# Kernel tuning notes

Measured on AMD Instinct MI355X. Metric: run time of the kernel, lower is better.

The kernel has to match this reference:

```python
import jax, jax.numpy as jnp
import numpy as np

B, S, T, E, H = 64, 256, 128, 256, 512


def setup_inputs() -> dict:
    key = jax.random.key(0)
    ks = jax.random.split(key, 12)
    sc = 0.05
    return {
        "trg_embed": jax.random.normal(ks[0], (B, T + 1, E), jnp.float32),
        "encoder_hidden": jax.random.normal(ks[1], (B, S, 2 * H), jnp.float32),
        "encoder_final": jax.random.normal(ks[2], (B, H), jnp.float32),
        "src_mask": jnp.ones((B, S), bool),
        "W_ih": jax.random.normal(ks[3], (3 * H, E + 2 * H), jnp.float32) * sc,
        "W_hh": jax.random.normal(ks[4], (3 * H, H), jnp.float32) * sc,
        "b_ih": jnp.zeros((3 * H,), jnp.float32),
        "b_hh": jnp.zeros((3 * H,), jnp.float32),
        "bridge_w": jax.random.normal(ks[5], (H, H), jnp.float32) * sc,
        "bridge_b": jnp.zeros((H,), jnp.float32),
        "key_w": jax.random.normal(ks[6], (H, 2 * H), jnp.float32) * sc,
        "query_w": jax.random.normal(ks[7], (H, H), jnp.float32) * sc,
        "energy_w": jax.random.normal(ks[8], (H,), jnp.float32) * sc,
        "pre_w": jax.random.normal(ks[9], (2 * H, H + 2 * H + E), jnp.float32) * sc,
        "pre_b": jnp.zeros((2 * H,), jnp.float32),
        "max_len": T,
    }


def reference(trg_embed, encoder_hidden, encoder_final, src_mask,
              W_ih, W_hh, b_ih, b_hh, bridge_w, bridge_b,
              key_w, query_w, energy_w, pre_w, pre_b, max_len):
    # bridge: initial decoder state from final encoder state
    h0 = jnp.tanh(encoder_final @ bridge_w.T + bridge_b)          # [B,H]
    # precomputed attention keys
    proj_key = jnp.einsum('bsk,hk->bsh', encoder_hidden, key_w)   # [B,S,H]
    neg = jnp.asarray(-1e9, trg_embed.dtype)

    prev = jnp.swapaxes(trg_embed[:, :max_len], 0, 1)             # [T,B,E]
    curr = jnp.swapaxes(trg_embed[:, 1:max_len + 1], 0, 1)        # [T,B,E] (generate_first)

    def step(h, pc):
        p, c = pc
        # --- additive (Bahdanau) attention, query = current hidden ---
        q = h @ query_w.T                                         # [B,H]
        scores = jnp.tanh(q[:, None, :] + proj_key) @ energy_w    # [B,S]
        scores = jnp.where(src_mask, scores, neg)
        alphas = jax.nn.softmax(scores, axis=-1)                  # [B,S]
        context = jnp.einsum('bs,bsd->bd', alphas, encoder_hidden)  # [B,2H]
        # --- generate_first: pre_output from previous hidden ---
        pre_out = jnp.concatenate([p, h, context], axis=-1) @ pre_w.T + pre_b  # [B,2H]
        # --- GRU cell (torch gate order r, z, n) ---
        x = jnp.concatenate([c, context], axis=-1)                # [B,E+2H]
        gi = x @ W_ih.T + b_ih
        gh = h @ W_hh.T + b_hh
        ir, iz, inn = jnp.split(gi, 3, axis=-1)
        hr, hz, hn = jnp.split(gh, 3, axis=-1)
        r = jax.nn.sigmoid(ir + hr)
        z = jax.nn.sigmoid(iz + hz)
        n = jnp.tanh(inn + r * hn)
        h_new = (1 - z) * n + z * h
        return h_new, (h_new, pre_out, alphas)

    h_fin, (states, pre_outs, attns) = jax.lax.scan(step, h0, (prev, curr))
    return (jnp.swapaxes(states, 0, 1),      # [B,T,H] decoder_states
            h_fin,                            # [B,H] final hidden
            jnp.swapaxes(pre_outs, 0, 1),     # [B,T,2H] pre_output_vectors
            jnp.swapaxes(attns, 0, 1))        # [B,T,S] attention_vectors
```

## Files before the change

### kernel.cpp

```cpp
#include <hip/hip_runtime.h>
#include <hip/hip_fp16.h>

using u32 = unsigned int;

constexpr int B = 64, S = 256, T = 128, E = 256, H = 512, H2 = 1024;
constexpr int TE = (T + 1) * E;

constexpr size_t OUT_HFIN = (size_t)B * T * H;
constexpr size_t OUT_PRE  = OUT_HFIN + (size_t)B * H;
constexpr size_t OUT_ATT  = OUT_PRE + (size_t)B * T * H2;

constexpr size_t WS_HPREV = 0;
constexpr size_t WS_QWT4  = 32768;
constexpr size_t WS_TRGT  = WS_QWT4 + 131072;
constexpr size_t WS_PK2   = WS_TRGT + 1056768;
constexpr size_t WS_HT2R  = WS_PK2 + 4194304;
constexpr size_t WS_QBUF  = WS_HT2R + 129 * 16384;
constexpr size_t WS_CTXR  = WS_QBUF + (size_t)128 * 16384;
constexpr size_t WS_SEWR  = WS_CTXR + (size_t)128 * 32768;
constexpr size_t WS_BAR   = WS_SEWR + 32768;
constexpr size_t WS_WFR   = WS_BAR + 1024;
constexpr size_t WS_TOTAL = WS_WFR + (size_t)192 * 3584 * 4;

constexpr int L_EHS  = 0;
constexpr int L_EW   = 131072;
constexpr int L_HP   = 133376;
constexpr int L_SH2  = 134400;
constexpr int L_QRED = 135424;
constexpr int L_SHQ  = 135424;
constexpr int L_SCP  = 137728;
constexpr int L_SE   = 142080;
constexpr int L_CPAR = 142336;
constexpr int L_CRE1 = 135424;
constexpr int L_CRC  = 139520;
constexpr int L_SST  = 151808;
constexpr int SMEM_BYTES = 155904;

typedef _Float16 half8 __attribute__((ext_vector_type(8)));
typedef float    f32x4 __attribute__((ext_vector_type(4)));
union UH  { u32 u; _Float16 h[2]; };
union UH8 { uint4 v; half8 h; };

__device__ __forceinline__ u32 pkh(float a, float b) {
  auto v = __builtin_amdgcn_cvt_pkrtz(a, b);
  u32 r; __builtin_memcpy(&r, &v, 4); return r;
}
__device__ __forceinline__ float f16lo(u32 u) { UH x; x.u = u; return (float)x.h[0]; }
__device__ __forceinline__ float f16hi(u32 u) { UH x; x.u = u; return (float)x.h[1]; }

#if __has_builtin(__builtin_amdgcn_fdot2)
__device__ __forceinline__ float fdot2(u32 a, u32 b, float c) {
  typedef _Float16 h2t __attribute__((ext_vector_type(2)));
  h2t av, bv; __builtin_memcpy(&av, &a, 4); __builtin_memcpy(&bv, &b, 4);
  return __builtin_amdgcn_fdot2(av, bv, c, false);
}
#else
__device__ __forceinline__ float fdot2(u32 a, u32 b, float c) {
  return c + f16lo(a) * f16lo(b) + f16hi(a) * f16hi(b);
}
#endif

__device__ __forceinline__ float fast_tanh(float x) {
  return 1.0f - 2.0f / (__expf(2.0f * x) + 1.0f);
}
__device__ __forceinline__ float fast_sigmoid(float x) {
  return 1.0f / (1.0f + __expf(-x));
}
__device__ __forceinline__ float dot4(float4 a, float4 b) {
  return a.x * b.x + a.y * b.y + a.z * b.z + a.w * b.w;
}

__device__ __forceinline__ void st_wt(u32* p, u32 v) {
  __hip_atomic_store(p, v, __ATOMIC_RELAXED, __HIP_MEMORY_SCOPE_AGENT);
}
__device__ __forceinline__ void st_wt_f(float* p, float v) {
  union { float f; u32 u; } c; c.f = v;
  __hip_atomic_store((u32*)p, c.u, __ATOMIC_RELAXED, __HIP_MEMORY_SCOPE_AGENT);
}

__device__ __forceinline__ void gbar(u32* bar, int p, u32 n) {
  asm volatile("s_waitcnt vmcnt(0) lgkmcnt(0)" ::: "memory");
  __syncthreads();
  if (threadIdx.x == 0) {
    u32 old = __hip_atomic_fetch_add(bar + (p >> 4) * 32, 1u,
                                     __ATOMIC_RELAXED, __HIP_MEMORY_SCOPE_AGENT);
    if ((old & 15u) == 15u) {
      u32 r = __hip_atomic_fetch_add(bar + 768, 1u,
                                     __ATOMIC_RELAXED, __HIP_MEMORY_SCOPE_AGENT);
      if ((r & 15u) == 15u)
        __hip_atomic_store(bar + 800, n, __ATOMIC_RELAXED, __HIP_MEMORY_SCOPE_AGENT);
    }
    while (__hip_atomic_load(bar + 800, __ATOMIC_RELAXED,
                             __HIP_MEMORY_SCOPE_AGENT) < n)
      __builtin_amdgcn_s_sleep(2);
  }
  __syncthreads();
  asm volatile("" ::: "memory");
}

__global__ void bridge_kernel(const float* __restrict__ ef,
                              const float* __restrict__ bw,
                              const float* __restrict__ bb,
                              float* __restrict__ h0T) {
  int gid = blockIdx.x * blockDim.x + threadIdx.x;
  int j = gid >> 6, b = gid & 63;
  const float4* w = (const float4*)(bw + (size_t)j * H);
  const float4* e = (const float4*)(ef + (size_t)b * H);
  float acc = 0.f;
#pragma unroll 4
  for (int k = 0; k < H / 4; ++k) acc += dot4(w[k], e[k]);
  h0T[gid] = tanhf(acc + bb[j]);
}

__global__ void packh0_kernel(const float* __restrict__ hprevT, u32* __restrict__ hT2) {
  int idx = blockIdx.x * 512 + threadIdx.x;
  int dp = idx >> 6, b = idx & 63;
  hT2[(size_t)(dp >> 2) * 256 + b * 4 + (dp & 3)] =
      pkh(hprevT[(size_t)(2 * dp) * 64 + b], hprevT[(size_t)(2 * dp + 1) * 64 + b]);
}

__global__ void qwt4_kernel(const float* __restrict__ qw, uint4* __restrict__ qwt4) {
  int kq = blockIdx.x, j = threadIdx.x;
  const float* src = qw + (size_t)j * H + kq * 8;
  uint4 o;
  o.x = pkh(src[0], src[1]); o.y = pkh(src[2], src[3]);
  o.z = pkh(src[4], src[5]); o.w = pkh(src[6], src[7]);
  qwt4[(size_t)kq * 512 + j] = o;
}

__global__ void trgT2_kernel(const float* __restrict__ trg, u32* __restrict__ trgT) {
  int b = blockIdx.x, tid = threadIdx.x;
  for (int i = 0; i < 33; ++i) {
    int idx = i * 512 + tid;
    if (idx >= 129 * 128) break;
    int tt = idx >> 7, kp = idx & 127;
    float2 v = *(const float2*)(trg + (size_t)b * TE + (size_t)tt * 256 + kp * 2);
    trgT[(size_t)tt * 8192 + (size_t)(kp >> 2) * 256 + b * 4 + (kp & 3)] = pkh(v.x, v.y);
  }
}

__global__ void wfrag_kernel(const float* __restrict__ W_ih,
                             const float* __restrict__ W_hh,
                             const float* __restrict__ pre_w,
                             uint4* __restrict__ wfr) {
  const int p = blockIdx.x;
  const bool isGate = p < 128;
  for (int idx = threadIdx.x; idx < 56 * 64; idx += 512) {
    int ks = idx >> 6, lane = idx & 63;
    u32 w4[4];
#pragma unroll
    for (int i = 0; i < 4; ++i) {
      int kp = ks * 16 + (lane >> 4) * 4 + i;
      float a = 0.f, bv = 0.f;
      if (isGate) {
        int row = lane & 15, jo = row >> 2, g = row & 3;
        int j = p * 4 + jo;
        if (kp < 128) {
          if (g < 3) { const float* s_ = W_ih + (size_t)(g * 512 + j) * 1280 + kp * 2; a = s_[0]; bv = s_[1]; }
        } else if (kp < 384) {
          int c = (kp - 128) * 2;
          if (g < 2)       { const float* s_ = W_hh + (size_t)(g * 512 + j) * 512 + c; a = s_[0]; bv = s_[1]; }
          else if (g == 3) { const float* s_ = W_hh + (size_t)(1024 + j) * 512 + c;    a = s_[0]; bv = s_[1]; }
        } else {
          if (g < 3) { const float* s_ = W_ih + (size_t)(g * 512 + j) * 1280 + 256 + (kp - 384) * 2; a = s_[0]; bv = s_[1]; }
        }
      } else {
        int row = (p - 128) * 16 + (lane & 15);
        int c = (kp < 128) ? kp * 2 : (kp < 384) ? 256 + (kp - 128) * 2 : 768 + (kp - 384) * 2;
        const float* s_ = pre_w + (size_t)row * 1792 + c;
        a = s_[0]; bv = s_[1];
      }
      w4[i] = pkh(a, bv);
    }
    wfr[(size_t)p * 3584 + idx] = make_uint4(w4[0], w4[1], w4[2], w4[3]);
  }
}

__global__ void __launch_bounds__(256, 4) projkey2_kernel(
    const float* __restrict__ eh, const float* __restrict__ key_w,
    u32* __restrict__ pk) {
  constexpr int ST = 68;
  __shared__ float ea[64][ST];
  __shared__ float kb[64][ST];
  const int b  = blockIdx.x;
  const int s0 = blockIdx.y * 64;
  const int j0 = blockIdx.z * 64;
  const int tid = threadIdx.x;
  const int rl = tid >> 2, ql = tid & 3;
  const int tx = tid & 15, ty = tid >> 4;
  float acc[4][4] = {};
  const float* esrc = eh + ((size_t)b * S + s0 + rl) * H2;
  const float* ksrc = key_w + (size_t)(j0 + rl) * H2;
  for (int kc = 0; kc < H2; kc += 64) {
    float4 ev[4], kv[4];
#pragma unroll
    for (int m = 0; m < 4; ++m) {
      ev[m] = *(const float4*)(esrc + kc + ql * 16 + m * 4);
      kv[m] = *(const float4*)(ksrc + kc + ql * 16 + m * 4);
    }
    __syncthreads();
#pragma unroll
    for (int m = 0; m < 4; ++m) {
#pragma unroll
      for (int c = 0; c < 4; ++c) {
        int k = ql * 16 + m * 4 + c;
        ea[k][rl] = (&ev[m].x)[c];
        kb[k][rl] = (&kv[m].x)[c];
      }
    }
    __syncthreads();
#pragma unroll 8
    for (int k = 0; k < 64; ++k) {
      float4 a4 = *(const float4*)&ea[k][ty * 4];
      float4 b4 = *(const float4*)&kb[k][tx * 4];
      float av[4] = {a4.x, a4.y, a4.z, a4.w};
      float bv[4] = {b4.x, b4.y, b4.z, b4.w};
#pragma unroll
      for (int i = 0; i < 4; ++i)
#pragma unroll
        for (int jj = 0; jj < 4; ++jj) acc[i][jj] += av[i] * bv[jj];
    }
  }
#pragma unroll
  for (int i = 0; i < 4; ++i) {
    int s = s0 + ty * 4 + i;
    u32 u0 = pkh(acc[i][0], acc[i][1]);
    u32 u1 = pkh(acc[i][2], acc[i][3]);
    *(uint2*)(pk + (size_t)(b * S + s) * 256 + j0 / 2 + tx * 2) = make_uint2(u0, u1);
  }
}

#define MFMA_STEP(k, bsrc, kq, acc) do {                                      \
    UH8 a_, b_;                                                               \
    a_.v = wfp[(size_t)(k) * 64];                                             \
    b_.v = *(const uint4*)((bsrc) + (size_t)(((kq) * 4 + g4) * 256 + bcol * 4)); \
    (acc) = __builtin_amdgcn_mfma_f32_16x16x32_f16(a_.h, b_.h, (acc), 0, 0, 0); \
  } while (0)

__global__ void __launch_bounds__(1024) decoder_loop(
    const float* __restrict__ eh,
    const float* __restrict__ b_ih, const float* __restrict__ b_hh,
    const float* __restrict__ energy_w, const float* __restrict__ pre_b,
    float* __restrict__ out, float* __restrict__ ws) {
  __builtin_amdgcn_fence(__ATOMIC_ACQUIRE, "agent");

  extern __shared__ char smem[];
  u32*   ehs  = (u32*)(smem + L_EHS);
  float* ew2  = (float*)(smem + L_EW);
  float* shp  = (float*)(smem + L_HP);
  u32*   sh2  = (u32*)(smem + L_SH2);
  float* qred = (float*)(smem + L_QRED);
  float* shq  = (float*)(smem + L_SHQ);
  float* scp  = (float*)(smem + L_SCP);
  float* sse  = (float*)(smem + L_SE);
  float* cpar = (float*)(smem + L_CPAR);
  float* cre1 = (float*)(smem + L_CRE1);
  float* crc  = (float*)(smem + L_CRC);
  float* sst  = (float*)(smem + L_SST);

  const uint4* qwt4 = (const uint4*)(ws + WS_QWT4);
  const u32* trgT = (const u32*)(ws + WS_TRGT);
  const u32* pk2  = (const u32*)(ws + WS_PK2);
  const uint4* wfru = (const uint4*)(ws + WS_WFR);
  u32*   ht2r = (u32*)(ws + WS_HT2R);
  u32*   qbr  = (u32*)(ws + WS_QBUF);
  u32*   ctxr = (u32*)(ws + WS_CTXR);
  float* sewr = ws + WS_SEWR;
  u32*   bar  = (u32*)(ws + WS_BAR);

  const int p = blockIdx.x, tid = threadIdx.x;
  const int lane = tid & 63, wid = tid >> 6;
  const int b = p >> 2, sib = p & 3, s0 = sib * 64;
  const int bt = wid & 3, kseg = wid >> 2;
  const int bcol = bt * 16 + (lane & 15);
  const int g4 = lane >> 4;

  for (int idx = tid; idx < 64 * 512; idx += 1024) {
    int s = idx >> 9, dp = idx & 511;
    float2 v = *(const float2*)(eh + (size_t)(b * 256 + s0 + s) * 1024 + 2 * dp);
    ehs[idx] = pkh(v.x, v.y);
  }
  if (tid < 512) ew2[(tid >> 5) * 36 + (tid & 31)] = energy_w[tid];
  if (p < 128 && tid < 256) {
    int jo = tid >> 6, b2 = tid & 63;
    shp[tid] = ws[WS_HPREV + (size_t)(p * 4 + jo) * 64 + b2];
  }
  u32 pkr[16];
  {
    const u32* pq = pk2 + (size_t)(b * 256 + s0 + (tid >> 4)) * 256 + (tid & 15) * 16;
#pragma unroll
    for (int i = 0; i < 16; ++i) pkr[i] = pq[i];
#pragma unroll
    for (int i = 0; i < 16; ++i) asm volatile("" : "+v"(pkr[i]));
  }
  __syncthreads();

  u32 bid = 0;
  for (int t = 0; t < T; ++t) {
    u32* ht2c = ht2r + (size_t)t * 16384;
    u32* ht2n = ht2r + (size_t)(t + 1) * 16384;
    u32* qbt  = qbr + (size_t)t * 16384;
    u32* ctxt = ctxr + (size_t)t * 32768;

    if (t > 0 && tid < 64) {
      float4 sv = *(const float4*)(sewr + (size_t)(t - 1) * 256 + (b << 2));
      float rinv = 1.f / (sv.x + sv.y + sv.z + sv.w);
      out[OUT_ATT + ((size_t)b * T + (t - 1)) * 256 + s0 + tid] *= rinv;
    }
    if (tid < 256)
      sh2[tid] = ht2c[(size_t)(tid >> 2) * 256 + b * 4 + (tid & 3)];
    __syncthreads();
    {
      const int jl = tid & 127, ks8 = tid >> 7;
      const int j = sib * 128 + jl;
      float acc = 0.f;
#pragma unroll
      for (int kk = 0; kk < 8; ++kk) {
        int kq = ks8 * 8 + kk;
        uint4 w = qwt4[(size_t)kq * 512 + j];
        acc = fdot2(w.x, sh2[kq * 4 + 0], acc);
        acc = fdot2(w.y, sh2[kq * 4 + 1], acc);
        acc = fdot2(w.z, sh2[kq * 4 + 2], acc);
        acc = fdot2(w.w, sh2[kq * 4 + 3], acc);
      }
      qred[jl * 8 + ks8] = acc;
    }
    __syncthreads();
    if (tid < 64) {
      float q0 = 0.f, q1 = 0.f;
#pragma unroll
      for (int i = 0; i < 8; ++i) { q0 += qred[(2 * tid) * 8 + i]; q1 += qred[(2 * tid + 1) * 8 + i]; }
      st_wt(qbt + (size_t)b * 256 + sib * 64 + tid, pkh(q0, q1));
    }
    gbar(bar, p, ++bid);

    if (tid < 256) {
      u32 qv = qbt[(size_t)b * 256 + tid];
      int j0 = 2 * tid;
      shq[(j0 >> 5) * 36 + (j0 & 31)] = f16lo(qv);
      shq[(j0 >> 5) * 36 + ((j0 & 31) + 1)] = f16hi(qv);
    }
    __syncthreads();
    {
      const int s = tid >> 4, jo = tid & 15;
      const float* q8 = shq + jo * 36;
      const float* e8 = ew2 + jo * 36;
      float acc = 0.f;
#pragma unroll
      for (int i = 0; i < 4; ++i) {
        const float* qq = q8 + i * 8;
        const float* ee = e8 + i * 8;
#pragma unroll
        for (int c = 0; c < 4; ++c) {
          u32 w = pkr[i * 4 + c];
          acc += fast_tanh(qq[2 * c] + f16lo(w)) * ee[2 * c] +
                 fast_tanh(qq[2 * c + 1] + f16hi(w)) * ee[2 * c + 1];
        }
      }
      scp[s * 17 + jo] = acc;
    }
    __syncthreads();
    if (tid < 64) {
      float sc = 0.f;
#pragma unroll
      for (int i = 0; i < 16; ++i) sc += scp[tid * 17 + i];
      float e = __expf(sc);
      out[OUT_ATT + ((size_t)b * T + t) * 256 + s0 + tid] = e;
      sse[tid] = e;
      float ssum = e;
      for (int d = 32; d; d >>= 1) ssum += __shfl_xor(ssum, d);
      if (tid == 0) st_wt_f(sewr + (size_t)t * 256 + p, ssum);
    }
    __syncthreads();
    {
      const int dp = tid & 511, sh = tid >> 9;
      float a0 = 0.f, a1 = 0.f;
      const u32* er = ehs + (sh * 32) * 512 + dp;
#pragma unroll 8
      for (int s = 0; s < 32; ++s) {
        u32 uu = er[s * 512];
        float es = sse[sh * 32 + s];
        a0 += es * f16lo(uu);
        a1 += es * f16hi(uu);
      }
      cpar[dp * 4 + sh * 2 + 0] = a0;
      cpar[dp * 4 + sh * 2 + 1] = a1;
    }
    __syncthreads();
    if (tid < 512) {
      float a0 = cpar[tid * 4 + 0] + cpar[tid * 4 + 2];
      float a1 = cpar[tid * 4 + 1] + cpar[tid * 4 + 3];
      __half2 v2 = __floats2half2_rn(a0, a1);
      unsafeAtomicAdd((__half2*)(ctxt + (size_t)(tid >> 2) * 256 + b * 4 + (tid & 3)), v2);
    }
    gbar(bar, p, ++bid);

    if (p < 192) {
      const bool isGate = p < 128;
      const u32* embB = trgT + (size_t)(isGate ? t + 1 : t) * 8192;
      const uint4* wfp = wfru + ((size_t)p * 56 + (size_t)kseg * 14) * 64 + lane;
      f32x4 ceh = {0.f, 0.f, 0.f, 0.f}, cct = {0.f, 0.f, 0.f, 0.f};
      if (kseg == 0) {
#pragma unroll
        for (int k = 0; k < 8; ++k) MFMA_STEP(k, embB, k, ceh);
#pragma unroll
        for (int k = 0; k < 6; ++k) MFMA_STEP(8 + k, ht2c, k, ceh);
      } else if (kseg == 1) {
#pragma unroll
        for (int k = 0; k < 10; ++k) MFMA_STEP(k, ht2c, 6 + k, ceh);
#pragma unroll
        for (int k = 0; k < 4; ++k) MFMA_STEP(10 + k, ctxt, k, cct);
      } else if (kseg == 2) {
#pragma unroll
        for (int k = 0; k < 14; ++k) MFMA_STEP(k, ctxt, 4 + k, cct);
      } else {
#pragma unroll
        for (int k = 0; k < 14; ++k) MFMA_STEP(k, ctxt, 18 + k, cct);
      }
      if (kseg != 0) {
        float* cc = crc + (size_t)((kseg - 1) * 256 + bt * 64 + lane) * 4;
        cc[0] = cct[0]; cc[1] = cct[1]; cc[2] = cct[2]; cc[3] = cct[3];
        if (kseg == 1) {
          float* ce = cre1 + (size_t)(bt * 64 + lane) * 4;
          ce[0] = ceh[0]; ce[1] = ceh[1]; ce[2] = ceh[2]; ce[3] = ceh[3];
        }
      }
      __syncthreads();
      if (kseg == 0) {
        const float* ce = cre1 + (size_t)(bt * 64 + lane) * 4;
        const float* c0 = crc + (size_t)(0 * 256 + bt * 64 + lane) * 4;
        const float* c1 = crc + (size_t)(1 * 256 + bt * 64 + lane) * 4;
        const float* c2 = crc + (size_t)(2 * 256 + bt * 64 + lane) * 4;
        float4 sv = *(const float4*)(sewr + (size_t)t * 256 + (bcol << 2));
        float rv = 1.f / (sv.x + sv.y + sv.z + sv.w);
        float eh0 = ceh[0] + ce[0], eh1 = ceh[1] + ce[1];
        float eh2_ = ceh[2] + ce[2], eh3 = ceh[3] + ce[3];
        float ct0 = (c0[0] + c1[0] + c2[0]) * rv;
        float ct1 = (c0[1] + c1[1] + c2[1]) * rv;
        float ct2 = (c0[2] + c1[2] + c2[2]) * rv;
        float ct3 = (c0[3] + c1[3] + c2[3]) * rv;
        if (isGate) {
          int j = p * 4 + g4;
          float r = fast_sigmoid(eh0 + ct0 + b_ih[j] + b_hh[j]);
          float z = fast_sigmoid(eh1 + ct1 + b_ih[512 + j] + b_hh[512 + j]);
          float n = fast_tanh((eh2_ + ct2 + b_ih[1024 + j]) +
                              r * (eh3 + b_hh[1024 + j]));
          float hp = shp[g4 * 64 + bcol];
          float hv = (1.f - z) * n + z * hp;
          shp[g4 * 64 + bcol] = hv;
          float ho = __shfl_xor(hv, 16);
          if ((g4 & 1) == 0) {
            int jp = p * 2 + (g4 >> 1);
            st_wt(ht2n + (size_t)(jp >> 2) * 256 + bcol * 4 + (jp & 3), pkh(hv, ho));
          }
          sst[g4 * 64 + bcol] = hv;
        } else {
          int prow = (p - 128) * 16 + g4 * 4;
          sst[(g4 * 4 + 0) * 64 + bcol] = eh0 + ct0 + pre_b[prow + 0];
          sst[(g4 * 4 + 1) * 64 + bcol] = eh1 + ct1 + pre_b[prow + 1];
          sst[(g4 * 4 + 2) * 64 + bcol] = eh2_ + ct2 + pre_b[prow + 2];
          sst[(g4 * 4 + 3) * 64 + bcol] = eh3 + ct3 + pre_b[prow + 3];
        }
      }
      __syncthreads();
      if (isGate) {
        if (tid < 64) {
          int b2 = tid;
          float4 o = make_float4(sst[0 * 64 + b2], sst[1 * 64 + b2],
                                 sst[2 * 64 + b2], sst[3 * 64 + b2]);
          *(float4*)(out + ((size_t)b2 * T + t) * 512 + p * 4) = o;
          if (t == T - 1)
            *(float4*)(out + OUT_HFIN + (size_t)b2 * 512 + p * 4) = o;
        }
      } else {
        if (tid < 256) {
          int b2 = tid & 63, q4 = tid >> 6;
          float4 o = make_float4(sst[(q4 * 4 + 0) * 64 + b2], sst[(q4 * 4 + 1) * 64 + b2],
                                 sst[(q4 * 4 + 2) * 64 + b2], sst[(q4 * 4 + 3) * 64 + b2]);
          *(float4*)(out + OUT_PRE + ((size_t)b2 * T + t) * 1024 + (p - 128) * 16 + q4 * 4) = o;
        }
      }
    }
    gbar(bar, p, ++bid);
  }

  if (tid < 64) {
    float4 sv = *(const float4*)(sewr + (size_t)(T - 1) * 256 + (b << 2));
    float rinv = 1.f / (sv.x + sv.y + sv.z + sv.w);
    out[OUT_ATT + ((size_t)b * T + (T - 1)) * 256 + s0 + tid] *= rinv;
  }
}

extern "C" void kernel_launch(void* const* d_in, const int* in_sizes, int n_in,
                              void* d_out, int out_size, void* d_ws, size_t ws_size,
                              hipStream_t stream) {
  const float* trg      = (const float*)d_in[0];
  const float* eh       = (const float*)d_in[1];
  const float* ef       = (const float*)d_in[2];
  const float* W_ih     = (const float*)d_in[4];
  const float* W_hh     = (const float*)d_in[5];
  const float* b_ih     = (const float*)d_in[6];
  const float* b_hh     = (const float*)d_in[7];
  const float* bridge_w = (const float*)d_in[8];
  const float* bridge_b = (const float*)d_in[9];
  const float* key_w    = (const float*)d_in[10];
  const float* query_w  = (const float*)d_in[11];
  const float* energy_w = (const float*)d_in[12];
  const float* pre_w    = (const float*)d_in[13];
  const float* pre_b    = (const float*)d_in[14];
  float* out = (float*)d_out;
  float* ws  = (float*)d_ws;

  hipMemsetAsync((char*)d_ws + WS_CTXR * sizeof(float), 0,
                 (WS_WFR - WS_CTXR) * sizeof(float), stream);
  bridge_kernel<<<64, 512, 0, stream>>>(ef, bridge_w, bridge_b, ws + WS_HPREV);
  packh0_kernel<<<32, 512, 0, stream>>>(ws + WS_HPREV, (u32*)(ws + WS_HT2R));
  qwt4_kernel<<<64, 512, 0, stream>>>(query_w, (uint4*)(ws + WS_QWT4));
  trgT2_kernel<<<64, 512, 0, stream>>>(trg, (u32*)(ws + WS_TRGT));
  wfrag_kernel<<<192, 512, 0, stream>>>(W_ih, W_hh, pre_w, (uint4*)(ws + WS_WFR));
  projkey2_kernel<<<dim3(B, S / 64, H / 64), 256, 0, stream>>>(eh, key_w,
                                                               (u32*)(ws + WS_PK2));

  hipFuncSetAttribute((const void*)decoder_loop,
                      hipFuncAttributeMaxDynamicSharedMemorySize, SMEM_BYTES);
  void* args[7];
  args[0] = (void*)&eh;
  args[1] = (void*)&b_ih;    args[2] = (void*)&b_hh;
  args[3] = (void*)&energy_w; args[4] = (void*)&pre_b;
  args[5] = (void*)&out;     args[6] = (void*)&ws;
  hipLaunchCooperativeKernel((const void*)decoder_loop, dim3(256), dim3(1024),
                             args, SMEM_BYTES, stream);
}
```

Baseline: 3.932 ms.

## Overlap attention with GRU matmuls, keep context weights in registers, flatten barrier

Restructures each decoder step. Attention scoring now uses half the waves with an intra-block atomic barrier, while the remaining waves compute the embedding and hidden-state MFMA products in the same phase, so that work moves off the post-barrier critical path. The context-weight fragment is loaded once into registers, and the block-to-batch mapping is permuted. The hierarchical grid barrier becomes a single flat counter, and the waves-per-EU attribute pins occupancy. Risks include register pressure from 64 extra live registers and contention on the single barrier atomic.

```diff
diff --git a/kernel.cpp b/kernel.cpp
--- a/kernel.cpp
+++ b/kernel.cpp
@@ -24,17 +24,15 @@
 
 constexpr int L_EHS  = 0;
 constexpr int L_EW   = 131072;
-constexpr int L_HP   = 133376;
-constexpr int L_SH2  = 134400;
-constexpr int L_QRED = 135424;
-constexpr int L_SHQ  = 135424;
-constexpr int L_SCP  = 137728;
-constexpr int L_SE   = 142080;
-constexpr int L_CPAR = 142336;
-constexpr int L_CRE1 = 135424;
-constexpr int L_CRC  = 139520;
-constexpr int L_SST  = 151808;
-constexpr int SMEM_BYTES = 155904;
+constexpr int L_HP   = 133184;
+constexpr int L_EBAR = 134208;
+constexpr int L_UNI  = 134272;
+constexpr int L_QRED = L_UNI;
+constexpr int L_SH2  = L_UNI + 4096;
+constexpr int L_SSE  = L_UNI;
+constexpr int L_CRC  = L_UNI;
+constexpr int L_SST  = L_UNI + 20480;
+constexpr int SMEM_BYTES = L_UNI + 24576;
 
 typedef _Float16 half8 __attribute__((ext_vector_type(8)));
 typedef float    f32x4 __attribute__((ext_vector_type(4)));
@@ -78,20 +76,17 @@
   __hip_atomic_store((u32*)p, c.u, __ATOMIC_RELAXED, __HIP_MEMORY_SCOPE_AGENT);
 }
 
-__device__ __forceinline__ void gbar(u32* bar, int p, u32 n) {
+__device__ __forceinline__ void gbar(u32* bar, u32 target) {
   asm volatile("s_waitcnt vmcnt(0) lgkmcnt(0)" ::: "memory");
   __syncthreads();
   if (threadIdx.x == 0) {
-    u32 old = __hip_atomic_fetch_add(bar + (p >> 4) * 32, 1u,
-                                     __ATOMIC_RELAXED, __HIP_MEMORY_SCOPE_AGENT);
-    if ((old & 15u) == 15u) {
-      u32 r = __hip_atomic_fetch_add(bar + 768, 1u,
-                                     __ATOMIC_RELAXED, __HIP_MEMORY_SCOPE_AGENT);
-      if ((r & 15u) == 15u)
-        __hip_atomic_store(bar + 800, n, __ATOMIC_RELAXED, __HIP_MEMORY_SCOPE_AGENT);
-    }
-    while (__hip_atomic_load(bar + 800, __ATOMIC_RELAXED,
-                             __HIP_MEMORY_SCOPE_AGENT) < n)
+    u32 old = __hip_atomic_fetch_add(bar, 1u, __ATOMIC_RELAXED,
+                                     __HIP_MEMORY_SCOPE_AGENT);
+    if (old == target - 1)
+      __hip_atomic_store(bar + 32, target, __ATOMIC_RELAXED,
+                         __HIP_MEMORY_SCOPE_AGENT);
+    while (__hip_atomic_load(bar + 32, __ATOMIC_RELAXED,
+                             __HIP_MEMORY_SCOPE_AGENT) < target)
       __builtin_amdgcn_s_sleep(2);
   }
   __syncthreads();
@@ -230,13 +225,7 @@
   }
 }
 
-#define MFMA_STEP(k, bsrc, kq, acc) do {                                      \
-    UH8 a_, b_;                                                               \
-    a_.v = wfp[(size_t)(k) * 64];                                             \
-    b_.v = *(const uint4*)((bsrc) + (size_t)(((kq) * 4 + g4) * 256 + bcol * 4)); \
-    (acc) = __builtin_amdgcn_mfma_f32_16x16x32_f16(a_.h, b_.h, (acc), 0, 0, 0); \
-  } while (0)
-
+__attribute__((amdgpu_waves_per_eu(4, 4)))
 __global__ void __launch_bounds__(1024) decoder_loop(
     const float* __restrict__ eh,
     const float* __restrict__ b_ih, const float* __restrict__ b_hh,
@@ -245,18 +234,15 @@
   __builtin_amdgcn_fence(__ATOMIC_ACQUIRE, "agent");
 
   extern __shared__ char smem[];
-  u32*   ehs  = (u32*)(smem + L_EHS);
-  float* ew2  = (float*)(smem + L_EW);
-  float* shp  = (float*)(smem + L_HP);
-  u32*   sh2  = (u32*)(smem + L_SH2);
-  float* qred = (float*)(smem + L_QRED);
-  float* shq  = (float*)(smem + L_SHQ);
-  float* scp  = (float*)(smem + L_SCP);
-  float* sse  = (float*)(smem + L_SE);
-  float* cpar = (float*)(smem + L_CPAR);
-  float* cre1 = (float*)(smem + L_CRE1);
-  float* crc  = (float*)(smem + L_CRC);
-  float* sst  = (float*)(smem + L_SST);
+  u32*   ehs   = (u32*)(smem + L_EHS);
+  float* ew2   = (float*)(smem + L_EW);
+  float* shp   = (float*)(smem + L_HP);
+  u32*   ebarp = (u32*)(smem + L_EBAR);
+  float* qred  = (float*)(smem + L_QRED);
+  u32*   sh2   = (u32*)(smem + L_SH2);
+  float* sse   = (float*)(smem + L_SSE);
+  float* crc   = (float*)(smem + L_CRC);
+  float* sst   = (float*)(smem + L_SST);
 
   const uint4* qwt4 = (const uint4*)(ws + WS_QWT4);
   const u32* trgT = (const u32*)(ws + WS_TRGT);
@@ -270,32 +256,45 @@
 
   const int p = blockIdx.x, tid = threadIdx.x;
   const int lane = tid & 63, wid = tid >> 6;
-  const int b = p >> 2, sib = p & 3, s0 = sib * 64;
+  const int b = (p & 7) * 8 + ((p >> 3) & 7), sib = p >> 6, s0 = sib * 64;
   const int bt = wid & 3, kseg = wid >> 2;
   const int bcol = bt * 16 + (lane & 15);
   const int g4 = lane >> 4;
-
+  const bool isG = p < 192, isGate = p < 128;
+
+  if (tid == 0) *ebarp = 0;
   for (int idx = tid; idx < 64 * 512; idx += 1024) {
     int s = idx >> 9, dp = idx & 511;
     float2 v = *(const float2*)(eh + (size_t)(b * 256 + s0 + s) * 1024 + 2 * dp);
     ehs[idx] = pkh(v.x, v.y);
   }
-  if (tid < 512) ew2[(tid >> 5) * 36 + (tid & 31)] = energy_w[tid];
-  if (p < 128 && tid < 256) {
+  if (tid < 512) ew2[(tid >> 6) * 66 + (tid & 63)] = energy_w[tid];
+  if (isGate && tid < 256) {
     int jo = tid >> 6, b2 = tid & 63;
     shp[tid] = ws[WS_HPREV + (size_t)(p * 4 + jo) * 64 + b2];
   }
-  u32 pkr[16];
-  {
-    const u32* pq = pk2 + (size_t)(b * 256 + s0 + (tid >> 4)) * 256 + (tid & 15) * 16;
-#pragma unroll
-    for (int i = 0; i < 16; ++i) pkr[i] = pq[i];
-#pragma unroll
-    for (int i = 0; i < 16; ++i) asm volatile("" : "+v"(pkr[i]));
-  }
+  u32 pkr[32] = {};
+  if (tid < 512) {
+    const u32* pq = pk2 + (size_t)(b * 256 + s0 + (tid >> 3)) * 256 + (tid & 7) * 32;
+#pragma unroll
+    for (int i = 0; i < 32; ++i) pkr[i] = pq[i];
+  }
+#pragma unroll
+  for (int i = 0; i < 32; ++i) asm volatile("" : "+v"(pkr[i]));
+  u32 wc[32] = {};
+  if (isG) {
+    const uint4* wp = wfru + ((size_t)p * 56 + 24 + (size_t)kseg * 8) * 64 + lane;
+#pragma unroll
+    for (int k = 0; k < 8; ++k) {
+      uint4 w = wp[(size_t)k * 64];
+      wc[4 * k] = w.x; wc[4 * k + 1] = w.y; wc[4 * k + 2] = w.z; wc[4 * k + 3] = w.w;
+    }
+  }
+#pragma unroll
+  for (int i = 0; i < 32; ++i) asm volatile("" : "+v"(wc[i]));
   __syncthreads();
 
-  u32 bid = 0;
+  u32 bid = 0, ebs = 0;
   for (int t = 0; t < T; ++t) {
     u32* ht2c = ht2r + (size_t)t * 16384;
     u32* ht2n = ht2r + (size_t)(t + 1) * 16384;
@@ -332,113 +331,100 @@
       for (int i = 0; i < 8; ++i) { q0 += qred[(2 * tid) * 8 + i]; q1 += qred[(2 * tid + 1) * 8 + i]; }
       st_wt(qbt + (size_t)b * 256 + sib * 64 + tid, pkh(q0, q1));
     }
-    gbar(bar, p, ++bid);
-
-    if (tid < 256) {
-      u32 qv = qbt[(size_t)b * 256 + tid];
-      int j0 = 2 * tid;
-      shq[(j0 >> 5) * 36 + (j0 & 31)] = f16lo(qv);
-      shq[(j0 >> 5) * 36 + ((j0 & 31) + 1)] = f16hi(qv);
-    }
-    __syncthreads();
-    {
-      const int s = tid >> 4, jo = tid & 15;
-      const float* q8 = shq + jo * 36;
-      const float* e8 = ew2 + jo * 36;
+    gbar(bar, 256 * ++bid);
+
+    f32x4 ceh = {0.f, 0.f, 0.f, 0.f};
+    if (tid < 512) {
+      const int s = tid >> 3, jo = tid & 7;
+      const u32* qrow = qbt + (size_t)b * 256 + jo * 32;
       float acc = 0.f;
 #pragma unroll
-      for (int i = 0; i < 4; ++i) {
-        const float* qq = q8 + i * 8;
-        const float* ee = e8 + i * 8;
+      for (int i = 0; i < 8; ++i) {
+        uint4 q4 = *(const uint4*)(qrow + i * 4);
+        const float* ee = ew2 + jo * 66 + i * 8;
 #pragma unroll
         for (int c = 0; c < 4; ++c) {
+          u32 qw = (&q4.x)[c];
           u32 w = pkr[i * 4 + c];
-          acc += fast_tanh(qq[2 * c] + f16lo(w)) * ee[2 * c] +
-                 fast_tanh(qq[2 * c + 1] + f16hi(w)) * ee[2 * c + 1];
+          acc += fast_tanh(f16lo(qw) + f16lo(w)) * ee[2 * c] +
+                 fast_tanh(f16hi(qw) + f16hi(w)) * ee[2 * c + 1];
         }
       }
-      scp[s * 17 + jo] = acc;
-    }
-    __syncthreads();
-    if (tid < 64) {
-      float sc = 0.f;
-#pragma unroll
-      for (int i = 0; i < 16; ++i) sc += scp[tid * 17 + i];
-      float e = __expf(sc);
-      out[OUT_ATT + ((size_t)b * T + t) * 256 + s0 + tid] = e;
-      sse[tid] = e;
-      float ssum = e;
-      for (int d = 32; d; d >>= 1) ssum += __shfl_xor(ssum, d);
-      if (tid == 0) st_wt_f(sewr + (size_t)t * 256 + p, ssum);
-    }
-    __syncthreads();
-    {
-      const int dp = tid & 511, sh = tid >> 9;
+      acc += __shfl_xor(acc, 1); acc += __shfl_xor(acc, 2); acc += __shfl_xor(acc, 4);
+      if (jo == 0) {
+        float e = __expf(acc);
+        out[OUT_ATT + ((size_t)b * T + t) * 256 + s0 + s] = e;
+        sse[s] = e;
+      }
+      ebs += 8;
+      if ((tid & 63) == 0)
+        __hip_atomic_fetch_add(ebarp, 1u, __ATOMIC_RELEASE, __HIP_MEMORY_SCOPE_WORKGROUP);
+      while (__hip_atomic_load(ebarp, __ATOMIC_ACQUIRE, __HIP_MEMORY_SCOPE_WORKGROUP) < ebs) {}
+      if (tid < 64) {
+        float sv = sse[tid];
+        for (int d = 32; d; d >>= 1) sv += __shfl_xor(sv, d);
+        if (tid == 0) st_wt_f(sewr + (size_t)t * 256 + b * 4 + sib, sv);
+      }
       float a0 = 0.f, a1 = 0.f;
-      const u32* er = ehs + (sh * 32) * 512 + dp;
+      const u32* er = ehs + tid;
 #pragma unroll 8
-      for (int s = 0; s < 32; ++s) {
-        u32 uu = er[s * 512];
-        float es = sse[sh * 32 + s];
+      for (int s2 = 0; s2 < 64; ++s2) {
+        u32 uu = er[s2 * 512];
+        float es = sse[s2];
         a0 += es * f16lo(uu);
         a1 += es * f16hi(uu);
       }
-      cpar[dp * 4 + sh * 2 + 0] = a0;
-      cpar[dp * 4 + sh * 2 + 1] = a1;
-    }
-    __syncthreads();
-    if (tid < 512) {
-      float a0 = cpar[tid * 4 + 0] + cpar[tid * 4 + 2];
-      float a1 = cpar[tid * 4 + 1] + cpar[tid * 4 + 3];
       __half2 v2 = __floats2half2_rn(a0, a1);
       unsafeAtomicAdd((__half2*)(ctxt + (size_t)(tid >> 2) * 256 + b * 4 + (tid & 3)), v2);
-    }
-    gbar(bar, p, ++bid);
-
-    if (p < 192) {
-      const bool isGate = p < 128;
+    } else if (isG) {
+      const int ea = kseg - 2;
       const u32* embB = trgT + (size_t)(isGate ? t + 1 : t) * 8192;
-      const uint4* wfp = wfru + ((size_t)p * 56 + (size_t)kseg * 14) * 64 + lane;
-      f32x4 ceh = {0.f, 0.f, 0.f, 0.f}, cct = {0.f, 0.f, 0.f, 0.f};
-      if (kseg == 0) {
-#pragma unroll
-        for (int k = 0; k < 8; ++k) MFMA_STEP(k, embB, k, ceh);
-#pragma unroll
-        for (int k = 0; k < 6; ++k) MFMA_STEP(8 + k, ht2c, k, ceh);
-      } else if (kseg == 1) {
-#pragma unroll
-        for (int k = 0; k < 10; ++k) MFMA_STEP(k, ht2c, 6 + k, ceh);
-#pragma unroll
-        for (int k = 0; k < 4; ++k) MFMA_STEP(10 + k, ctxt, k, cct);
-      } else if (kseg == 2) {
-#pragma unroll
-        for (int k = 0; k < 14; ++k) MFMA_STEP(k, ctxt, 4 + k, cct);
-      } else {
-#pragma unroll
-        for (int k = 0; k < 14; ++k) MFMA_STEP(k, ctxt, 18 + k, cct);
+      const uint4* wp = wfru + ((size_t)p * 56 + (size_t)ea * 12) * 64 + lane;
+#pragma unroll
+      for (int k = 0; k < 12; ++k) {
+        int ks = ea * 12 + k;
+        const u32* bsrc; int kq;
+        if (ks < 8) { bsrc = embB; kq = ks; } else { bsrc = ht2c; kq = ks - 8; }
+        UH8 a_, b_;
+        a_.v = wp[(size_t)k * 64];
+        b_.v = *(const uint4*)(bsrc + (size_t)((kq * 4 + g4) * 256 + bcol * 4));
+        ceh = __builtin_amdgcn_mfma_f32_16x16x32_f16(a_.h, b_.h, ceh, 0, 0, 0);
+      }
+    }
+    gbar(bar, 256 * ++bid);
+
+    if (isG) {
+      f32x4 cct = {0.f, 0.f, 0.f, 0.f};
+#pragma unroll
+      for (int k = 0; k < 8; ++k) {
+        UH8 a_, b_;
+        a_.v = make_uint4(wc[4 * k], wc[4 * k + 1], wc[4 * k + 2], wc[4 * k + 3]);
+        b_.v = *(const uint4*)(ctxt + (size_t)(((kseg * 8 + k) * 4 + g4) * 256 + bcol * 4));
+        cct = __builtin_amdgcn_mfma_f32_16x16x32_f16(a_.h, b_.h, cct, 0, 0, 0);
       }
       if (kseg != 0) {
         float* cc = crc + (size_t)((kseg - 1) * 256 + bt * 64 + lane) * 4;
         cc[0] = cct[0]; cc[1] = cct[1]; cc[2] = cct[2]; cc[3] = cct[3];
-        if (kseg == 1) {
-          float* ce = cre1 + (size_t)(bt * 64 + lane) * 4;
-          ce[0] = ceh[0]; ce[1] = ceh[1]; ce[2] = ceh[2]; ce[3] = ceh[3];
-        }
+      }
+      if (wid >= 8) {
+        float* ce = crc + (size_t)((3 + (kseg - 2)) * 256 + bt * 64 + lane) * 4;
+        ce[0] = ceh[0]; ce[1] = ceh[1]; ce[2] = ceh[2]; ce[3] = ceh[3];
       }
       __syncthreads();
       if (kseg == 0) {
-        const float* ce = cre1 + (size_t)(bt * 64 + lane) * 4;
         const float* c0 = crc + (size_t)(0 * 256 + bt * 64 + lane) * 4;
         const float* c1 = crc + (size_t)(1 * 256 + bt * 64 + lane) * 4;
         const float* c2 = crc + (size_t)(2 * 256 + bt * 64 + lane) * 4;
+        const float* e0 = crc + (size_t)(3 * 256 + bt * 64 + lane) * 4;
+        const float* e1 = crc + (size_t)(4 * 256 + bt * 64 + lane) * 4;
         float4 sv = *(const float4*)(sewr + (size_t)t * 256 + (bcol << 2));
         float rv = 1.f / (sv.x + sv.y + sv.z + sv.w);
-        float eh0 = ceh[0] + ce[0], eh1 = ceh[1] + ce[1];
-        float eh2_ = ceh[2] + ce[2], eh3 = ceh[3] + ce[3];
-        float ct0 = (c0[0] + c1[0] + c2[0]) * rv;
-        float ct1 = (c0[1] + c1[1] + c2[1]) * rv;
-        float ct2 = (c0[2] + c1[2] + c2[2]) * rv;
-        float ct3 = (c0[3] + c1[3] + c2[3]) * rv;
+        float eh0 = e0[0] + e1[0], eh1 = e0[1] + e1[1];
+        float eh2_ = e0[2] + e1[2], eh3 = e0[3] + e1[3];
+        float ct0 = (cct[0] + c0[0] + c1[0] + c2[0]) * rv;
+        float ct1 = (cct[1] + c0[1] + c1[1] + c2[1]) * rv;
+        float ct2 = (cct[2] + c0[2] + c1[2] + c2[2]) * rv;
+        float ct3 = (cct[3] + c0[3] + c1[3] + c2[3]) * rv;
         if (isGate) {
           int j = p * 4 + g4;
           float r = fast_sigmoid(eh0 + ct0 + b_ih[j] + b_hh[j]);
@@ -481,7 +467,7 @@
         }
       }
     }
-    gbar(bar, p, ++bid);
+    gbar(bar, 256 * ++bid);
   }
 
   if (tid < 64) {
```

New measurement: 5.041 ms. +28.2%, slower.
